# Kernel optimization log

Hardware: AMD Instinct MI355X
Metric: run time of the kernel (lower is better)

Reference implementation:

```python
import jax, jax.numpy as jnp
import numpy as np

WEIGHT = 1.0  # init kwarg
B, N, M, D = 32, 128, 128, 256


def _hungarian(cost):
    """O(n^3) Hungarian (Jonker-Volgenant potentials form) on host numpy.
    cost: [n, m] with n <= m. Returns col index assigned to each row
    (row_ind is implicitly arange(n), matching scipy.linear_sum_assignment).
    """
    cost = np.asarray(cost, dtype=np.float64)
    n, m = cost.shape
    u = np.zeros(n + 1)
    v = np.zeros(m + 1)
    p = np.zeros(m + 1, dtype=np.int64)   # p[j] = row (1-based) matched to col j
    way = np.zeros(m + 1, dtype=np.int64)
    for i in range(1, n + 1):
        p[0] = i
        j0 = 0
        minv = np.full(m + 1, np.inf)
        used = np.zeros(m + 1, dtype=bool)
        while True:
            used[j0] = True
            i0 = p[j0]
            free = ~used[1:]
            cur = cost[i0 - 1, :] - u[i0] - v[1:]
            upd = free & (cur < minv[1:])
            minv[1:][upd] = cur[upd]
            way[1:][upd] = j0
            masked = np.where(free, minv[1:], np.inf)
            j1 = int(np.argmin(masked)) + 1
            delta = masked[j1 - 1]
            u[p[used]] += delta
            v[used] -= delta
            minv[1:][free] -= delta
            j0 = j1
            if p[j0] == 0:
                break
        while j0:
            j1 = way[j0]
            p[j0] = p[j1]
            j0 = j1
    col_of_row = np.zeros(n, dtype=np.int64)
    for j in range(1, m + 1):
        if p[j] > 0:
            col_of_row[p[j] - 1] = j - 1
    return col_of_row


def _pairwise_mse(p, g):
    """cost[b,i,j] = mean_d (p[b,i,d]-g[b,j,d])^2, fused without [B,N,M,D] tensor."""
    d = p.shape[-1]
    p2 = jnp.sum(p * p, axis=-1)                    # [B,N]
    g2 = jnp.sum(g * g, axis=-1)                    # [B,M]
    pg = jnp.einsum('bnd,bmd->bnm', p, g)           # [B,N,M]
    return (p2[:, :, None] + g2[:, None, :] - 2.0 * pg) / d


def setup_inputs() -> dict:
    key = jax.random.key(0)
    k1, k2 = jax.random.split(key)
    batch_prediction = jax.random.normal(k1, (B, N, D), dtype=jnp.float32)
    batch_groundtruth = jax.random.normal(k2, (B, M, D), dtype=jnp.float32)
    return {"batch_prediction": batch_prediction,
            "batch_groundtruth": batch_groundtruth}


def reference(batch_prediction, batch_groundtruth):
    b, n = batch_prediction.shape[0], batch_prediction.shape[1]
    cost = _pairwise_mse(batch_prediction, batch_groundtruth)   # [B,N,M]
    cost_np = np.asarray(jax.device_get(cost))
    # Hungarian assignment on host (matches scipy.linear_sum_assignment; CPU-bound)
    cols = jnp.asarray(np.stack([_hungarian(cost_np[bi]) for bi in range(b)]))  # [B,N]
    matched = cost[jnp.arange(b)[:, None], jnp.arange(n)[None, :], cols]        # [B,N]
    loss = matched.mean(axis=1).sum() / b * WEIGHT
    return jnp.reshape(loss, (1,))
```

## Files before the change

kernel.cpp:

```cpp
#include <hip/hip_runtime.h>
#include <float.h>

#define Bc 32
#define Nn 128
#define Dd 256

__global__ __launch_bounds__(64) void cost_kernel(const float* __restrict__ P,
                                                  const float* __restrict__ G,
                                                  float* __restrict__ C) {
    const int b = blockIdx.y;
    const int i = blockIdx.x;
    const int t = threadIdx.x;

    const float4 pv = ((const float4*)(P + ((size_t)b * Nn + i) * Dd))[t];
    const float4* g4 = (const float4*)(G + (size_t)b * Nn * Dd);
    float* crow = C + ((size_t)b * Nn + i) * Nn;

    for (int j = 0; j < Nn; j += 2) {
        float4 gv0 = g4[(size_t)j * 64 + t];
        float4 gv1 = g4[(size_t)(j + 1) * 64 + t];
        float dx0 = pv.x - gv0.x, dy0 = pv.y - gv0.y, dz0 = pv.z - gv0.z, dw0 = pv.w - gv0.w;
        float dx1 = pv.x - gv1.x, dy1 = pv.y - gv1.y, dz1 = pv.z - gv1.z, dw1 = pv.w - gv1.w;
        float s0 = dx0 * dx0 + dy0 * dy0 + dz0 * dz0 + dw0 * dw0;
        float s1 = dx1 * dx1 + dy1 * dy1 + dz1 * dz1 + dw1 * dw1;
#pragma unroll
        for (int off = 32; off; off >>= 1) {
            s0 += __shfl_xor(s0, off);
            s1 += __shfl_xor(s1, off);
        }
        if (t == 0) {
            crow[j]     = s0 * (1.0f / (float)Dd);
            crow[j + 1] = s1 * (1.0f / (float)Dd);
        }
    }
}

template <int CTRL>
__device__ __forceinline__ float dpp_movf(float x) {
    return __int_as_float(__builtin_amdgcn_update_dpp(
        0x7f7fffff , __float_as_int(x), CTRL,
        0xf, 0xf, false));
}

__device__ __forceinline__ float wave_min_lane63(float x) {
    x = fminf(x, dpp_movf<0x121>(x));
    x = fminf(x, dpp_movf<0x122>(x));
    x = fminf(x, dpp_movf<0x124>(x));
    x = fminf(x, dpp_movf<0x128>(x));
    x = fminf(x, dpp_movf<0x142>(x));
    x = fminf(x, dpp_movf<0x143>(x));
    return x;
}

template <int CTRL>
__device__ __forceinline__ void dpp2min_step(float& m1, float& m2) {
    float o1 = dpp_movf<CTRL>(m1);
    float o2 = dpp_movf<CTRL>(m2);
    float n1 = fminf(m1, o1);
    m2 = fminf(fmaxf(m1, o1), fminf(m2, o2));
    m1 = n1;
}

__device__ __forceinline__ float readlane_f(float v, int lane) {
    return __int_as_float(__builtin_amdgcn_readlane(__float_as_int(v), lane));
}

__global__ __launch_bounds__(64) void hungarian_kernel(const float* __restrict__ Call,
                                                       float* __restrict__ out) {
    const int b = blockIdx.x;
    const int t = threadIdx.x;

    __shared__ float Csh[Nn * Nn];
    __shared__ int claim[Nn];

    {
        const float4* src = (const float4*)(Call + (size_t)b * Nn * Nn);
        float4* dst = (float4*)Csh;
#pragma unroll
        for (int k = 0; k < (Nn * Nn / 4) / 64; ++k)
            dst[k * 64 + t] = src[k * 64 + t];
    }
    claim[t] = 0x7fffffff;
    claim[t + 64] = 0x7fffffff;
    __syncthreads();

    float bestA = FLT_MAX, bestB = FLT_MAX;
    int argA = 0, argB = 0;
    for (int i = 0; i < Nn; ++i) {
        float c0 = Csh[i * Nn + t];
        float c1 = Csh[i * Nn + t + 64];
        if (c0 < bestA) { bestA = c0; argA = i; }
        if (c1 < bestB) { bestB = c1; argB = i; }
    }
    float vA = bestA, vB = bestB;
    atomicMin(&claim[argA], t);
    atomicMin(&claim[argB], t + 64);
    __syncthreads();

    float uA = 0.0f, uB = 0.0f;
    float wA = 0.0f, wB = 0.0f;
    int pA = 0, pB = 0;
    if (claim[argA] == t)      pA = argA + 1;
    if (claim[argB] == t + 64) pB = argB + 1;

    unsigned long long fmA = __ballot(claim[t] == 0x7fffffff);
    unsigned long long fmB = __ballot(claim[t + 64] == 0x7fffffff);

    for (int pass = 0; pass < 2; ++pass) {
        if (!(fmA | fmB)) break;
        unsigned long long remA = fmA, remB = fmB;
        int guard = 0;
        while ((remA | remB) != 0ull && guard++ < 256) {
            int l, i, slotR;
            if (remA) { l = __ffsll(remA) - 1; remA &= remA - 1; i = l + 1;  slotR = 0;
                        if (!((fmA >> l) & 1)) continue; }
            else      { l = __ffsll(remB) - 1; remB &= remB - 1; i = l + 65; slotR = 1;
                        if (!((fmB >> l) & 1)) continue; }

            const float* crow = &Csh[(i - 1) * Nn];
            float cur0 = crow[t] - vA;
            float cur1 = crow[t + 64] - vB;
            float m1 = fminf(cur0, cur1);
            float m2 = fmaxf(cur0, cur1);
            dpp2min_step<0x121>(m1, m2);
            dpp2min_step<0x122>(m1, m2);
            dpp2min_step<0x124>(m1, m2);
            dpp2min_step<0x128>(m1, m2);
            dpp2min_step<0x142>(m1, m2);
            dpp2min_step<0x143>(m1, m2);
            float s_m1 = readlane_f(m1, 63);
            float s_m2 = readlane_f(m2, 63);

            unsigned long long b0 = __ballot(cur0 == s_m1);
            unsigned long long b1 = __ballot(cur1 == s_m1);
            int j1 = b0 ? __ffsll(b0) : (__ffsll(b1) + 64);
            int lane1 = (j1 - 1) & 63, slot1 = (j1 - 1) >> 6;

            if (t == l) { if (slotR == 0) uA = s_m2; else uB = s_m2; }

            int k0 = __builtin_amdgcn_readlane(slot1 ? pB : pA, lane1);
            bool strict = (s_m1 < s_m2);
            if (!strict && k0 != 0) continue;

            if (t == lane1) {
                if (slot1 == 0) { vA += s_m1 - s_m2; pA = i; wA = s_m2; }
                else            { vB += s_m1 - s_m2; pB = i; wB = s_m2; }
            }
            if (slotR == 0) fmA &= ~(1ull << l); else fmB &= ~(1ull << l);
            if (k0 != 0) {
                int kl = (k0 - 1) & 63;
                if (k0 <= 64) { fmA |= 1ull << kl; remA |= 1ull << kl; }
                else          { fmB |= 1ull << kl; remB |= 1ull << kl; }
            }
        }
    }

    for (int slotR = 0; slotR < 2; ++slotR) {
        unsigned long long mask = slotR ? fmB : fmA;
        while (mask) {
            int l = __ffsll(mask) - 1;
            mask &= mask - 1;
            int i = l + 1 + slotR * 64;

            float minvA = FLT_MAX, minvB = FLT_MAX;
            int wayA = 0, wayB = 0;
            bool usedA = false, usedB = false;
            bool rUA = false, rUB = false;
            if (t == l) { if (slotR == 0) rUA = true; else rUB = true; }

            int s_j0 = 0;
            int s_i0 = i;
            float s_u = readlane_f(slotR ? uB : uA, l);
            int s_j1;

            for (;;) {
                const float* crow = &Csh[(s_i0 - 1) * Nn];
                float c0 = crow[t];
                float c1 = crow[t + 64];
                if (!usedA) {
                    float cur = c0 - s_u - vA;
                    if (cur < minvA) { minvA = cur; wayA = s_j0; }
                }
                if (!usedB) {
                    float cur = c1 - s_u - vB;
                    if (cur < minvB) { minvB = cur; wayB = s_j0; }
                }

                float mA = usedA ? FLT_MAX : minvA;
                float mB = usedB ? FLT_MAX : minvB;
                float r63 = wave_min_lane63(fminf(mA, mB));
                float s_delta = readlane_f(r63, 63);
                unsigned long long ba = __ballot(mA == s_delta);
                unsigned long long bb = __ballot(mB == s_delta);
                s_j1 = ba ? __ffsll(ba) : (__ffsll(bb) + 64);

                if (usedA) { vA -= s_delta; wA += s_delta; } else { minvA -= s_delta; }
                if (usedB) { vB -= s_delta; wB += s_delta; } else { minvB -= s_delta; }
                if (rUA) uA += s_delta;
                if (rUB) uB += s_delta;

                int lane1 = (s_j1 - 1) & 63;
                int slot1 = (s_j1 - 1) >> 6;
                int s_p = __builtin_amdgcn_readlane(slot1 ? pB : pA, lane1);
                float s_w = readlane_f(slot1 ? wB : wA, lane1);

                if (s_p == 0) break;

                if (t == lane1) { if (slot1 == 0) usedA = true; else usedB = true; }
                {
                    int r = s_p - 1;
                    if (t == (r & 63)) { if ((r >> 6) == 0) rUA = true; else rUB = true; }
                }
                s_j0 = s_j1;
                s_i0 = s_p;
                s_u = s_w;
            }

            int s_j = s_j1;
            while (s_j) {
                int lane = (s_j - 1) & 63;
                int slot = (s_j - 1) >> 6;
                int s_jprev = __builtin_amdgcn_readlane(slot ? wayB : wayA, lane);
                int s_pnew;
                if (s_jprev == 0) {
                    s_pnew = i;
                } else {
                    int lp = (s_jprev - 1) & 63;
                    int sp = (s_jprev - 1) >> 6;
                    s_pnew = __builtin_amdgcn_readlane(sp ? pB : pA, lp);
                }
                int rl = (s_pnew - 1) & 63;
                int rs = (s_pnew - 1) >> 6;
                float s_unew = readlane_f(rs ? uB : uA, rl);
                if (t == lane) {
                    if (slot == 0) { pA = s_pnew; wA = s_unew; }
                    else           { pB = s_pnew; wB = s_unew; }
                }
                s_j = s_jprev;
            }
        }
    }

    float tot = Csh[(pA - 1) * Nn + t] + Csh[(pB - 1) * Nn + t + 64];
#pragma unroll
    for (int off = 32; off; off >>= 1) tot += __shfl_xor(tot, off);

    if (t == 0) {
        atomicAdd(out, tot * (1.0f / ((float)Nn * (float)Bc)));
    }
}

extern "C" void kernel_launch(void* const* d_in, const int* in_sizes, int n_in,
                              void* d_out, int out_size, void* d_ws, size_t ws_size,
                              hipStream_t stream) {
    const float* P = (const float*)d_in[0];
    const float* G = (const float*)d_in[1];
    float* out = (float*)d_out;
    float* C = (float*)d_ws;

    (void)hipMemsetAsync(out, 0, sizeof(float), stream);

    dim3 gcost(Nn, Bc);
    cost_kernel<<<gcost, 64, 0, stream>>>(P, G, C);
    hungarian_kernel<<<Bc, 64, 0, stream>>>(C, out);
}
```

Before: 626.5 us.

## Pack min key with index, prefetch next cost row, use DPP sums, drop memset

The Hungarian inner loop now packs each candidate's minv and column index into one unsigned key, so a single DPP unsigned-min reduction replaces the float min plus two ballots. The next cost row is loaded from shared memory before the dual updates, which hides LDS latency across iterations. The cost-kernel and final sums use DPP row reductions instead of shuffles, and the output zeroing moves into the cost kernel so the memset launch goes away. Truncating the low 8 mantissa bits of the key loses precision in delta and can change tie-breaking and the chosen assignment. Clamping reduced costs to zero also departs from the exact algorithm.

```diff
diff --git a/kernel.cpp b/kernel.cpp
--- a/kernel.cpp
+++ b/kernel.cpp
@@ -5,12 +5,63 @@
 #define Nn 128
 #define Dd 256
 
+template <int CTRL>
+__device__ __forceinline__ float dpp_addsrc(float x) {
+    return __int_as_float(__builtin_amdgcn_update_dpp(0, __float_as_int(x), CTRL,
+                                                      0xf, 0xf, false));
+}
+__device__ __forceinline__ float wave_sum_lane63(float x) {
+    x += dpp_addsrc<0x121>(x);
+    x += dpp_addsrc<0x122>(x);
+    x += dpp_addsrc<0x124>(x);
+    x += dpp_addsrc<0x128>(x);
+    x += dpp_addsrc<0x142>(x);
+    x += dpp_addsrc<0x143>(x);
+    return x;
+}
+
+template <int CTRL>
+__device__ __forceinline__ unsigned dpp_movu(unsigned x) {
+    return (unsigned)__builtin_amdgcn_update_dpp((int)0xFFFFFFFFu, (int)x, CTRL,
+                                                 0xf, 0xf, false);
+}
+__device__ __forceinline__ unsigned wave_umin_lane63(unsigned x) {
+    x = min(x, dpp_movu<0x121>(x));
+    x = min(x, dpp_movu<0x122>(x));
+    x = min(x, dpp_movu<0x124>(x));
+    x = min(x, dpp_movu<0x128>(x));
+    x = min(x, dpp_movu<0x142>(x));
+    x = min(x, dpp_movu<0x143>(x));
+    return x;
+}
+
+template <int CTRL>
+__device__ __forceinline__ float dpp_movf(float x) {
+    return __int_as_float(__builtin_amdgcn_update_dpp(0x7f7fffff, __float_as_int(x),
+                                                      CTRL, 0xf, 0xf, false));
+}
+template <int CTRL>
+__device__ __forceinline__ void dpp2min_step(float& m1, float& m2) {
+    float o1 = dpp_movf<CTRL>(m1);
+    float o2 = dpp_movf<CTRL>(m2);
+    float n1 = fminf(m1, o1);
+    m2 = fminf(fmaxf(m1, o1), fminf(m2, o2));
+    m1 = n1;
+}
+
+__device__ __forceinline__ float readlane_f(float v, int lane) {
+    return __int_as_float(__builtin_amdgcn_readlane(__float_as_int(v), lane));
+}
+
 __global__ __launch_bounds__(64) void cost_kernel(const float* __restrict__ P,
                                                   const float* __restrict__ G,
-                                                  float* __restrict__ C) {
+                                                  float* __restrict__ C,
+                                                  float* __restrict__ out) {
     const int b = blockIdx.y;
     const int i = blockIdx.x;
     const int t = threadIdx.x;
+
+    if (b == 0 && i == 0 && t == 0) *out = 0.0f;
 
     const float4 pv = ((const float4*)(P + ((size_t)b * Nn + i) * Dd))[t];
     const float4* g4 = (const float4*)(G + (size_t)b * Nn * Dd);
@@ -23,46 +74,13 @@
         float dx1 = pv.x - gv1.x, dy1 = pv.y - gv1.y, dz1 = pv.z - gv1.z, dw1 = pv.w - gv1.w;
         float s0 = dx0 * dx0 + dy0 * dy0 + dz0 * dz0 + dw0 * dw0;
         float s1 = dx1 * dx1 + dy1 * dy1 + dz1 * dz1 + dw1 * dw1;
-#pragma unroll
-        for (int off = 32; off; off >>= 1) {
-            s0 += __shfl_xor(s0, off);
-            s1 += __shfl_xor(s1, off);
-        }
-        if (t == 0) {
+        s0 = wave_sum_lane63(s0);
+        s1 = wave_sum_lane63(s1);
+        if (t == 63) {
             crow[j]     = s0 * (1.0f / (float)Dd);
             crow[j + 1] = s1 * (1.0f / (float)Dd);
         }
     }
-}
-
-template <int CTRL>
-__device__ __forceinline__ float dpp_movf(float x) {
-    return __int_as_float(__builtin_amdgcn_update_dpp(
-        0x7f7fffff , __float_as_int(x), CTRL,
-        0xf, 0xf, false));
-}
-
-__device__ __forceinline__ float wave_min_lane63(float x) {
-    x = fminf(x, dpp_movf<0x121>(x));
-    x = fminf(x, dpp_movf<0x122>(x));
-    x = fminf(x, dpp_movf<0x124>(x));
-    x = fminf(x, dpp_movf<0x128>(x));
-    x = fminf(x, dpp_movf<0x142>(x));
-    x = fminf(x, dpp_movf<0x143>(x));
-    return x;
-}
-
-template <int CTRL>
-__device__ __forceinline__ void dpp2min_step(float& m1, float& m2) {
-    float o1 = dpp_movf<CTRL>(m1);
-    float o2 = dpp_movf<CTRL>(m2);
-    float n1 = fminf(m1, o1);
-    m2 = fminf(fmaxf(m1, o1), fminf(m2, o2));
-    m1 = n1;
-}
-
-__device__ __forceinline__ float readlane_f(float v, int lane) {
-    return __int_as_float(__builtin_amdgcn_readlane(__float_as_int(v), lane));
 }
 
 __global__ __launch_bounds__(64) void hungarian_kernel(const float* __restrict__ Call,
@@ -169,41 +187,47 @@
             if (t == l) { if (slotR == 0) rUA = true; else rUB = true; }
 
             int s_j0 = 0;
-            int s_i0 = i;
             float s_u = readlane_f(slotR ? uB : uA, l);
             int s_j1;
 
+            float c0 = Csh[(i - 1) * Nn + t];
+            float c1 = Csh[(i - 1) * Nn + t + 64];
+
             for (;;) {
-                const float* crow = &Csh[(s_i0 - 1) * Nn];
-                float c0 = crow[t];
-                float c1 = crow[t + 64];
                 if (!usedA) {
-                    float cur = c0 - s_u - vA;
+                    float cur = fmaxf(c0 - s_u - vA, 0.0f);
                     if (cur < minvA) { minvA = cur; wayA = s_j0; }
                 }
                 if (!usedB) {
-                    float cur = c1 - s_u - vB;
+                    float cur = fmaxf(c1 - s_u - vB, 0.0f);
                     if (cur < minvB) { minvB = cur; wayB = s_j0; }
                 }
 
-                float mA = usedA ? FLT_MAX : minvA;
-                float mB = usedB ? FLT_MAX : minvB;
-                float r63 = wave_min_lane63(fminf(mA, mB));
-                float s_delta = readlane_f(r63, 63);
-                unsigned long long ba = __ballot(mA == s_delta);
-                unsigned long long bb = __ballot(mB == s_delta);
-                s_j1 = ba ? __ffsll(ba) : (__ffsll(bb) + 64);
-
-                if (usedA) { vA -= s_delta; wA += s_delta; } else { minvA -= s_delta; }
-                if (usedB) { vB -= s_delta; wB += s_delta; } else { minvB -= s_delta; }
-                if (rUA) uA += s_delta;
-                if (rUB) uB += s_delta;
+                unsigned kA = (__float_as_uint(usedA ? FLT_MAX : minvA) & 0xFFFFFF00u)
+                              | (unsigned)t;
+                unsigned kB = (__float_as_uint(usedB ? FLT_MAX : minvB) & 0xFFFFFF00u)
+                              | (unsigned)(t + 64);
+                unsigned k = wave_umin_lane63(min(kA, kB));
+                unsigned s_key = (unsigned)__builtin_amdgcn_readlane((int)k, 63);
+                float s_delta = __uint_as_float(s_key & 0xFFFFFF00u);
+                s_j1 = (int)(s_key & 0xFFu) + 1;
 
                 int lane1 = (s_j1 - 1) & 63;
                 int slot1 = (s_j1 - 1) >> 6;
                 int s_p = __builtin_amdgcn_readlane(slot1 ? pB : pA, lane1);
                 float s_w = readlane_f(slot1 ? wB : wA, lane1);
 
+                int nrow = (s_p > 0 ? s_p : 1) - 1;
+                float nc0 = Csh[nrow * Nn + t];
+                float nc1 = Csh[nrow * Nn + t + 64];
+
+                if (usedA) { vA -= s_delta; wA += s_delta; }
+                else       { minvA = fmaxf(minvA - s_delta, 0.0f); }
+                if (usedB) { vB -= s_delta; wB += s_delta; }
+                else       { minvB = fmaxf(minvB - s_delta, 0.0f); }
+                if (rUA) uA += s_delta;
+                if (rUB) uB += s_delta;
+
                 if (s_p == 0) break;
 
                 if (t == lane1) { if (slot1 == 0) usedA = true; else usedB = true; }
@@ -212,8 +236,9 @@
                     if (t == (r & 63)) { if ((r >> 6) == 0) rUA = true; else rUB = true; }
                 }
                 s_j0 = s_j1;
-                s_i0 = s_p;
                 s_u = s_w;
+                c0 = nc0;
+                c1 = nc1;
             }
 
             int s_j = s_j1;
@@ -242,10 +267,9 @@
     }
 
     float tot = Csh[(pA - 1) * Nn + t] + Csh[(pB - 1) * Nn + t + 64];
-#pragma unroll
-    for (int off = 32; off; off >>= 1) tot += __shfl_xor(tot, off);
-
-    if (t == 0) {
+    tot = wave_sum_lane63(tot);
+
+    if (t == 63) {
         atomicAdd(out, tot * (1.0f / ((float)Nn * (float)Bc)));
     }
 }
@@ -258,9 +282,7 @@
     float* out = (float*)d_out;
     float* C = (float*)d_ws;
 
-    (void)hipMemsetAsync(out, 0, sizeof(float), stream);
-
     dim3 gcost(Nn, Bc);
-    cost_kernel<<<gcost, 64, 0, stream>>>(P, G, C);
+    cost_kernel<<<gcost, 64, 0, stream>>>(P, G, C, out);
     hungarian_kernel<<<Bc, 64, 0, stream>>>(C, out);
 }
```

Result: faster. 548.9 us (-12.4%).
